# Performance work log

Measured on AMD Instinct MI355X. Metric: run time of the kernel, lower is better.

Reference implementation:

```python
import jax, jax.numpy as jnp
import numpy as np

B, C, CE, H, W = 4, 128, 64, 64, 64
V = H * W
# parent(i) < i//2 guarantees depth <= ceil(log2(V)) = 12; 14 is a safe static bound
MAX_LEVELS = 14


def _gather_v(x, idx):
    # x: [B, C, V], idx: [B, V] -> gather along vertex dim (broadcast over C)
    return jnp.take_along_axis(x, idx[:, None, :], axis=2)


def _tree_filter(feature_in, embed_in, sorted_index, sorted_parent, node_level):
    Bv, Cv, Hv, Wv = feature_in.shape
    Vv = Hv * Wv
    f = feature_in.reshape(Bv, Cv, Vv)
    e = embed_in.reshape(Bv, embed_in.shape[1], Vv)
    # build_edge_weight: gather to BFS order, gather parent, squared-L2 distance, exp(-d)
    f_s = _gather_v(f, sorted_index)          # [B,C,V] features in topological order
    e_s = _gather_v(e, sorted_index)
    e_p = _gather_v(e_s, sorted_parent)
    d2 = jnp.sum((e_s - e_p) ** 2, axis=1)    # [B,V]
    w = jnp.exp(-d2)                          # edge weight node->parent (root: exp(0)=1, unused)
    wB = w[:, None, :]
    # ---- up sweep (leaves -> root), level-parallel over BFS levels ----
    # A_i = f_i + sum_{c in child(i)} w_c * A_c ; Z_i = 1 + sum w_c * Z_c (self_weight = 1)
    aggr_up = f_s
    nrm_up = jnp.ones((Bv, Vv), feature_in.dtype)
    for d in range(MAX_LEVELS - 1, 0, -1):
        mw = jnp.where(node_level == d, w, jnp.zeros((), feature_in.dtype))
        aggr_up = jax.vmap(lambda a, p, m: a.at[:, p].add(m))(
            aggr_up, sorted_parent, mw[:, None, :] * aggr_up)
        nrm_up = jax.vmap(lambda a, p, m: a.at[p].add(m))(
            nrm_up, sorted_parent, mw * nrm_up)
    # ---- down sweep (root -> leaves) ----
    # Ahat_i = A_i + w_i * (Ahat_parent - w_i * A_i); root keeps A_root
    aggr = aggr_up
    nrm = nrm_up
    for d in range(1, MAX_LEVELS):
        sel = node_level == d
        pa = _gather_v(aggr, sorted_parent)
        aggr = jnp.where(sel[:, None, :], aggr_up + wB * (pa - wB * aggr_up), aggr)
        pn = jnp.take_along_axis(nrm, sorted_parent, axis=1)
        nrm = jnp.where(sel, nrm_up + w * (pn - w * nrm_up), nrm)
    out_s = aggr / nrm[:, None, :]
    # scatter back from BFS order to original vertex order
    out = jax.vmap(lambda o, i: jnp.zeros_like(o).at[:, i].set(o))(out_s, sorted_index)
    return out.reshape(Bv, Cv, Hv, Wv)


def setup_inputs() -> dict:
    key = jax.random.key(0)
    k1, k2 = jax.random.split(key)
    feature_in = jax.random.normal(k1, (B, C, H, W), dtype=jnp.float32)
    embed_in = 0.1 * jax.random.normal(k2, (B, CE, H, W), dtype=jnp.float32)
    rng = np.random.default_rng(0)
    sorted_index = np.stack([rng.permutation(V) for _ in range(B)]).astype(np.int32)
    sorted_parent = np.zeros((B, V), dtype=np.int32)
    node_level = np.zeros((B, V), dtype=np.int32)
    for b in range(B):
        for i in range(1, V):
            p = int(rng.integers(0, max(1, i // 2)))  # parent earlier in order, depth <= log2(V)
            sorted_parent[b, i] = p
            node_level[b, i] = node_level[b, p] + 1
    return {
        "feature_in": feature_in,
        "embed_in": embed_in,
        "sorted_index": jnp.asarray(sorted_index),
        "sorted_parent": jnp.asarray(sorted_parent),
        "node_level": jnp.asarray(node_level),
    }


def reference(feature_in, embed_in, sorted_index, sorted_parent, node_level):
    return _tree_filter(feature_in, embed_in, sorted_index, sorted_parent, node_level)
```

## Files before the change

kernel.cpp:

```cpp
#include <hip/hip_runtime.h>

#define BB 4
#define CC 128
#define CE 64
#define VV 4096
#define NLEV 14

__global__ __launch_bounds__(256) void prep_kernel(
    const float* __restrict__ embed,
    const int*  __restrict__ sorted_index,
    const int*  __restrict__ sorted_parent,
    const int*  __restrict__ node_level,
    float* __restrict__ w_ws,
    int*   __restrict__ levelorder,
    int*   __restrict__ offsets)
{
    int tid = threadIdx.x;
    if (blockIdx.x < BB) {
        int b = blockIdx.x;
        __shared__ int hist[NLEV];
        __shared__ int base[NLEV + 1];
        __shared__ int cursor[NLEV];
        if (tid < NLEV) hist[tid] = 0;
        __syncthreads();
        for (int v = tid; v < VV; v += 256) {
            int d = node_level[b * VV + v];
            if (d >= 0 && d < NLEV) atomicAdd(&hist[d], 1);
        }
        __syncthreads();
        if (tid == 0) {
            int acc = 0;
            for (int d = 0; d < NLEV; ++d) { base[d] = acc; cursor[d] = acc; acc += hist[d]; }
            base[NLEV] = acc;
        }
        __syncthreads();
        for (int v = tid; v < VV; v += 256) {
            int d = node_level[b * VV + v];
            if (d >= 0 && d < NLEV) {
                int pos = atomicAdd(&cursor[d], 1);
                levelorder[b * VV + pos] = v;
            }
        }
        if (tid <= NLEV) offsets[b * 16 + tid] = base[tid];
    } else {
        int lane = tid & 63;
        int wv   = tid >> 6;
        long g = (long)(blockIdx.x - BB) * 4 + wv;
        if (g >= (long)BB * VV) return;
        int b = (int)(g >> 12);
        int i = (int)(g & (VV - 1));
        int vi = sorted_index[b * VV + i];
        int p  = sorted_parent[b * VV + i];
        int vp = sorted_index[b * VV + p];
        const float* eb = embed + (size_t)b * CE * VV;
        float diff = eb[(size_t)lane * VV + vi] - eb[(size_t)lane * VV + vp];
        float d2 = diff * diff;
        #pragma unroll
        for (int o = 32; o > 0; o >>= 1) d2 += __shfl_xor(d2, o, 64);
        if (lane == 0) w_ws[b * VV + i] = __expf(-d2);
    }
}

__global__ __launch_bounds__(256) void tree_kernel(
    const float* __restrict__ feat,
    const int*  __restrict__ sorted_index,
    const int*  __restrict__ sorted_parent,
    const float* __restrict__ w_ws,
    const int*  __restrict__ levelorder,
    const int*  __restrict__ offsets,
    float* __restrict__ out)
{
    __shared__ float val[VV];
    __shared__ float vn[VV];
    int blk = blockIdx.x;
    int b = blk / CC;
    int c = blk % CC;
    int tid = threadIdx.x;

    const int*   si  = sorted_index  + b * VV;
    const int*   par = sorted_parent + b * VV;
    const float* wb  = w_ws          + b * VV;
    const int*   lo  = levelorder    + b * VV;
    const int*   off = offsets       + b * 16;
    const float* f   = feat + ((size_t)b * CC + c) * VV;

    for (int v = tid; v < VV; v += 256) {
        val[v] = f[si[v]];
        vn[v]  = 1.0f;
    }
    __syncthreads();

    for (int d = NLEV - 1; d >= 1; --d) {
        int s = off[d], e = off[d + 1];
        for (int k = s + tid; k < e; k += 256) {
            int i = lo[k];
            int p = par[i];
            float wi = wb[i];
            atomicAdd(&val[p], wi * val[i]);
            atomicAdd(&vn[p],  wi * vn[i]);
        }
        __syncthreads();
    }

    for (int d = 1; d <= NLEV - 1; ++d) {
        int s = off[d], e = off[d + 1];
        for (int k = s + tid; k < e; k += 256) {
            int i = lo[k];
            int p = par[i];
            float wi = wb[i];
            float u  = val[i];
            float un = vn[i];
            val[i] = fmaf(wi, val[p] - wi * u,  u);
            vn[i]  = fmaf(wi, vn[p]  - wi * un, un);
        }
        __syncthreads();
    }

    float* ob = out + ((size_t)b * CC + c) * VV;
    for (int v = tid; v < VV; v += 256) {
        ob[si[v]] = val[v] / vn[v];
    }
}

extern "C" void kernel_launch(void* const* d_in, const int* in_sizes, int n_in,
                              void* d_out, int out_size, void* d_ws, size_t ws_size,
                              hipStream_t stream) {
    const float* feat          = (const float*)d_in[0];
    const float* embed         = (const float*)d_in[1];
    const int*   sorted_index  = (const int*)d_in[2];
    const int*   sorted_parent = (const int*)d_in[3];
    const int*   node_level    = (const int*)d_in[4];
    float* out = (float*)d_out;

    char* ws = (char*)d_ws;
    float* w_ws       = (float*)ws;
    int*   levelorder = (int*)(ws + (size_t)BB * VV * 4);
    int*   offsets    = (int*)(ws + (size_t)2 * BB * VV * 4);

    int wblocks = (BB * VV + 3) / 4;
    prep_kernel<<<BB + wblocks, 256, 0, stream>>>(
        embed, sorted_index, sorted_parent, node_level, w_ws, levelorder, offsets);

    tree_kernel<<<BB * CC, 256, 0, stream>>>(
        feat, sorted_index, sorted_parent, w_ws, levelorder, offsets, out);
}
```

Baseline: 126.9 us.

## Relabel tree nodes in level order and factor normalizer into separate pass

Nodes are renumbered into level-contiguous positions, with gather indices, parent positions and edge weights precomputed in that order, so the per-channel kernel reads contiguous arrays instead of chasing an indirection. The normalizer sweep, identical for every channel, moves into a small per-batch kernel that emits reciprocals, which drops one LDS array and half the atomics from the per-channel work. The per-channel kernel becomes a single 64-thread wave that replaces barriers with waitcnt and uses unsafe LDS float atomics. The trade-off is four launches instead of two, and less parallelism per block for the wide levels.

```diff
diff --git a/kernel.cpp b/kernel.cpp
--- a/kernel.cpp
+++ b/kernel.cpp
@@ -6,120 +6,149 @@
 #define VV 4096
 #define NLEV 14
 
-__global__ __launch_bounds__(256) void prep_kernel(
-    const float* __restrict__ embed,
-    const int*  __restrict__ sorted_index,
-    const int*  __restrict__ sorted_parent,
-    const int*  __restrict__ node_level,
-    float* __restrict__ w_ws,
-    int*   __restrict__ levelorder,
-    int*   __restrict__ offsets)
+
+__device__ __forceinline__ void lds_fadd(float* p, float v) {
+    unsafeAtomicAdd(p, v);
+}
+
+__global__ __launch_bounds__(256) void sort_kernel(
+    const int* __restrict__ sorted_index,
+    const int* __restrict__ sorted_parent,
+    const int* __restrict__ node_level,
+    int* __restrict__ gi,
+    int* __restrict__ cpk,
+    int* __restrict__ pos,
+    int* __restrict__ offs)
 {
-    int tid = threadIdx.x;
-    if (blockIdx.x < BB) {
-        int b = blockIdx.x;
-        __shared__ int hist[NLEV];
-        __shared__ int base[NLEV + 1];
-        __shared__ int cursor[NLEV];
-        if (tid < NLEV) hist[tid] = 0;
-        __syncthreads();
-        for (int v = tid; v < VV; v += 256) {
-            int d = node_level[b * VV + v];
-            if (d >= 0 && d < NLEV) atomicAdd(&hist[d], 1);
-        }
-        __syncthreads();
-        if (tid == 0) {
-            int acc = 0;
-            for (int d = 0; d < NLEV; ++d) { base[d] = acc; cursor[d] = acc; acc += hist[d]; }
-            base[NLEV] = acc;
-        }
-        __syncthreads();
-        for (int v = tid; v < VV; v += 256) {
-            int d = node_level[b * VV + v];
-            if (d >= 0 && d < NLEV) {
-                int pos = atomicAdd(&cursor[d], 1);
-                levelorder[b * VV + pos] = v;
-            }
-        }
-        if (tid <= NLEV) offsets[b * 16 + tid] = base[tid];
-    } else {
-        int lane = tid & 63;
-        int wv   = tid >> 6;
-        long g = (long)(blockIdx.x - BB) * 4 + wv;
-        if (g >= (long)BB * VV) return;
-        int b = (int)(g >> 12);
-        int i = (int)(g & (VV - 1));
-        int vi = sorted_index[b * VV + i];
-        int p  = sorted_parent[b * VV + i];
-        int vp = sorted_index[b * VV + p];
-        const float* eb = embed + (size_t)b * CE * VV;
-        float diff = eb[(size_t)lane * VV + vi] - eb[(size_t)lane * VV + vp];
-        float d2 = diff * diff;
-        #pragma unroll
-        for (int o = 32; o > 0; o >>= 1) d2 += __shfl_xor(d2, o, 64);
-        if (lane == 0) w_ws[b * VV + i] = __expf(-d2);
+    __shared__ int pos_s[VV];
+    __shared__ int hist[NLEV + 1];
+    __shared__ int cursor[NLEV];
+    int b = blockIdx.x, tid = threadIdx.x;
+    const int* lev = node_level   + b * VV;
+    const int* si  = sorted_index + b * VV;
+    const int* par = sorted_parent+ b * VV;
+
+    if (tid < NLEV + 1) hist[tid] = 0;
+    __syncthreads();
+    for (int i = tid; i < VV; i += 256) atomicAdd(&hist[lev[i]], 1);
+    __syncthreads();
+    if (tid == 0) {
+        int acc = 0;
+        for (int d = 0; d < NLEV; ++d) { int h = hist[d]; hist[d] = acc; cursor[d] = acc; acc += h; }
+        hist[NLEV] = acc;
+    }
+    __syncthreads();
+    if (tid <= NLEV) offs[b * 16 + tid] = hist[tid];
+    for (int i = tid; i < VV; i += 256) {
+        int k = atomicAdd(&cursor[lev[i]], 1);
+        pos_s[i] = k;
+        pos[b * VV + i] = k;
+        gi[b * VV + k] = si[i];
+    }
+    __syncthreads();
+    for (int i = tid; i < VV; i += 256) {
+        cpk[b * VV + pos_s[i]] = pos_s[par[i]];
     }
 }
 
-__global__ __launch_bounds__(256) void tree_kernel(
+__global__ __launch_bounds__(256) void weight_kernel(
+    const float* __restrict__ embed,
+    const int* __restrict__ sorted_index,
+    const int* __restrict__ sorted_parent,
+    const int* __restrict__ pos,
+    float* __restrict__ wl)
+{
+    int lane = threadIdx.x & 63;
+    int g = blockIdx.x * 4 + (threadIdx.x >> 6);
+    int b = g >> 12;
+    int i = g & (VV - 1);
+    int vi = sorted_index[b * VV + i];
+    int p  = sorted_parent[b * VV + i];
+    int vp = sorted_index[b * VV + p];
+    const float* eb = embed + (size_t)b * CE * VV;
+    float diff = eb[(size_t)lane * VV + vi] - eb[(size_t)lane * VV + vp];
+    float d2 = diff * diff;
+    #pragma unroll
+    for (int o = 32; o > 0; o >>= 1) d2 += __shfl_xor(d2, o, 64);
+    if (lane == 0) wl[b * VV + pos[b * VV + i]] = __expf(-d2);
+}
+
+__global__ __launch_bounds__(256) void nrm_kernel(
+    const int* __restrict__ cpk,
+    const float* __restrict__ wl,
+    const int* __restrict__ offs,
+    float* __restrict__ invnrm)
+{
+    __shared__ float vn[VV];
+    int b = blockIdx.x, tid = threadIdx.x;
+    const int*   cp  = cpk + b * VV;
+    const float* w   = wl  + b * VV;
+    const int*   off = offs+ b * 16;
+
+    for (int k = tid; k < VV; k += 256) vn[k] = 1.0f;
+    __syncthreads();
+    for (int d = NLEV - 1; d >= 1; --d) {
+        int e = off[d + 1];
+        for (int k = off[d] + tid; k < e; k += 256)
+            lds_fadd(&vn[cp[k]], w[k] * vn[k]);
+        __syncthreads();
+    }
+    for (int d = 1; d <= NLEV - 1; ++d) {
+        int e = off[d + 1];
+        for (int k = off[d] + tid; k < e; k += 256) {
+            float u = vn[k], wk = w[k];
+            vn[k] = fmaf(wk, vn[cp[k]] - wk * u, u);
+        }
+        __syncthreads();
+    }
+    for (int k = tid; k < VV; k += 256) invnrm[b * VV + k] = 1.0f / vn[k];
+}
+
+__global__ __launch_bounds__(64) void tree_kernel(
     const float* __restrict__ feat,
-    const int*  __restrict__ sorted_index,
-    const int*  __restrict__ sorted_parent,
-    const float* __restrict__ w_ws,
-    const int*  __restrict__ levelorder,
-    const int*  __restrict__ offsets,
+    const int* __restrict__ gi,
+    const int* __restrict__ cpk,
+    const float* __restrict__ wl,
+    const float* __restrict__ invnrm,
+    const int* __restrict__ offs,
     float* __restrict__ out)
 {
     __shared__ float val[VV];
-    __shared__ float vn[VV];
     int blk = blockIdx.x;
-    int b = blk / CC;
-    int c = blk % CC;
-    int tid = threadIdx.x;
+    int b = blk >> 7;
+    int c = blk & (CC - 1);
+    int lane = threadIdx.x;
 
-    const int*   si  = sorted_index  + b * VV;
-    const int*   par = sorted_parent + b * VV;
-    const float* wb  = w_ws          + b * VV;
-    const int*   lo  = levelorder    + b * VV;
-    const int*   off = offsets       + b * 16;
-    const float* f   = feat + ((size_t)b * CC + c) * VV;
+    const int*   g   = gi     + b * VV;
+    const int*   cp  = cpk    + b * VV;
+    const float* w   = wl     + b * VV;
+    const float* inr = invnrm + b * VV;
+    const int*   off = offs   + b * 16;
+    const float* f   = feat + ((size_t)(b * CC + c)) * VV;
 
-    for (int v = tid; v < VV; v += 256) {
-        val[v] = f[si[v]];
-        vn[v]  = 1.0f;
-    }
-    __syncthreads();
+    #pragma unroll 8
+    for (int k = lane; k < VV; k += 64) val[k] = f[g[k]];
+    __asm__ volatile("s_waitcnt lgkmcnt(0)" ::: "memory");
 
     for (int d = NLEV - 1; d >= 1; --d) {
-        int s = off[d], e = off[d + 1];
-        for (int k = s + tid; k < e; k += 256) {
-            int i = lo[k];
-            int p = par[i];
-            float wi = wb[i];
-            atomicAdd(&val[p], wi * val[i]);
-            atomicAdd(&vn[p],  wi * vn[i]);
-        }
-        __syncthreads();
+        int e = off[d + 1];
+        for (int k = off[d] + lane; k < e; k += 64)
+            lds_fadd(&val[cp[k]], w[k] * val[k]);
+        __asm__ volatile("s_waitcnt lgkmcnt(0)" ::: "memory");
     }
 
     for (int d = 1; d <= NLEV - 1; ++d) {
-        int s = off[d], e = off[d + 1];
-        for (int k = s + tid; k < e; k += 256) {
-            int i = lo[k];
-            int p = par[i];
-            float wi = wb[i];
-            float u  = val[i];
-            float un = vn[i];
-            val[i] = fmaf(wi, val[p] - wi * u,  u);
-            vn[i]  = fmaf(wi, vn[p]  - wi * un, un);
+        int e = off[d + 1];
+        for (int k = off[d] + lane; k < e; k += 64) {
+            float u = val[k], wk = w[k];
+            val[k] = fmaf(wk, val[cp[k]] - wk * u, u);
         }
-        __syncthreads();
+        __asm__ volatile("s_waitcnt lgkmcnt(0)" ::: "memory");
     }
 
-    float* ob = out + ((size_t)b * CC + c) * VV;
-    for (int v = tid; v < VV; v += 256) {
-        ob[si[v]] = val[v] / vn[v];
-    }
+    float* ob = out + ((size_t)(b * CC + c)) * VV;
+    #pragma unroll 4
+    for (int k = lane; k < VV; k += 64) ob[g[k]] = val[k] * inr[k];
 }
 
 extern "C" void kernel_launch(void* const* d_in, const int* in_sizes, int n_in,
@@ -133,14 +162,22 @@
     float* out = (float*)d_out;
 
     char* ws = (char*)d_ws;
-    float* w_ws       = (float*)ws;
-    int*   levelorder = (int*)(ws + (size_t)BB * VV * 4);
-    int*   offsets    = (int*)(ws + (size_t)2 * BB * VV * 4);
+    const size_t A = (size_t)BB * VV * 4;
+    int*   gi     = (int*)  (ws);
+    int*   cpk    = (int*)  (ws + A);
+    float* wl     = (float*)(ws + 2 * A);
+    void*  posnrm = (void*) (ws + 3 * A);
+    int*   offs   = (int*)  (ws + 4 * A);
 
-    int wblocks = (BB * VV + 3) / 4;
-    prep_kernel<<<BB + wblocks, 256, 0, stream>>>(
-        embed, sorted_index, sorted_parent, node_level, w_ws, levelorder, offsets);
+    sort_kernel<<<BB, 256, 0, stream>>>(
+        sorted_index, sorted_parent, node_level, gi, cpk, (int*)posnrm, offs);
 
-    tree_kernel<<<BB * CC, 256, 0, stream>>>(
-        feat, sorted_index, sorted_parent, w_ws, levelorder, offsets, out);
+    weight_kernel<<<(BB * VV) / 4, 256, 0, stream>>>(
+        embed, sorted_index, sorted_parent, (const int*)posnrm, wl);
+
+    nrm_kernel<<<BB, 256, 0, stream>>>(
+        cpk, wl, offs, (float*)posnrm);
+
+    tree_kernel<<<BB * CC, 64, 0, stream>>>(
+        feat, gi, cpk, wl, (const float*)posnrm, offs, out);
 }
```

Result: slower. 146.7 us (+15.6%).
